# Kernel tuning notes

Measured on AMD Instinct MI355X. Metric: run time of the kernel, lower is better.

## Reference

```python
import jax, jax.numpy as jnp
import numpy as np

N = 50000
E = 800000
HID = 128
EIN = 2 * HID + 1  # h[row] ++ h[col] ++ edge_attr
NC = 3             # n_coords
DIM = 3            # spatial dim
NORM_FACTOR = 100.0
LN_EPS = 1e-5


def layernorm(x, g, b):
    m = jnp.mean(x, axis=-1, keepdims=True)
    v = jnp.mean(jnp.square(x - m), axis=-1, keepdims=True)
    return (x - m) * jax.lax.rsqrt(v + LN_EPS) * g + b


def setup_inputs() -> dict:
    key = jax.random.key(0)
    ks = jax.random.split(key, 12)
    h = jax.random.normal(ks[0], (N, HID), dtype=jnp.float32)
    coord = jax.random.normal(ks[1], (N, NC, DIM), dtype=jnp.float32)
    coord_diff = jax.random.normal(ks[2], (E, NC, DIM), dtype=jnp.float32)
    edge_attr = jax.random.normal(ks[3], (E, 1), dtype=jnp.float32)
    edge_mask = jnp.ones((E, 1), dtype=jnp.float32)
    node_mask = jnp.ones((N, 1, 1), dtype=jnp.float32)
    row = jax.random.randint(ks[4], (E,), 0, N, dtype=jnp.int32)
    col = jax.random.randint(ks[5], (E,), 0, N, dtype=jnp.int32)
    # MLP params (stored [in, out])
    def xavier(k, fi, fo, gain=1.0):
        lim = gain * np.sqrt(6.0 / (fi + fo))
        return jax.random.uniform(k, (fi, fo), dtype=jnp.float32, minval=-lim, maxval=lim)
    W1 = xavier(ks[6], EIN, HID)
    b1 = jnp.zeros((HID,), jnp.float32)
    g1 = jnp.ones((HID,), jnp.float32)
    be1 = jnp.zeros((HID,), jnp.float32)
    W2 = xavier(ks[7], HID, HID)
    b2 = jnp.zeros((HID,), jnp.float32)
    g2 = jnp.ones((HID,), jnp.float32)
    be2 = jnp.zeros((HID,), jnp.float32)
    W3 = xavier(ks[8], HID, NC * NC, gain=0.01)  # final layer, no bias
    return dict(h=h, coord=coord, coord_diff=coord_diff, edge_attr=edge_attr,
                edge_mask=edge_mask, node_mask=node_mask, row=row, col=col,
                W1=W1, b1=b1, g1=g1, be1=be1, W2=W2, b2=b2, g2=g2, be2=be2, W3=W3)


def reference(h, coord, coord_diff, edge_attr, edge_mask, node_mask, row, col,
              W1, b1, g1, be1, W2, b2, g2, be2, W3):
    # gather node feats into edge features: [E, 2*HID + 1]
    x = jnp.concatenate([h[row], h[col], edge_attr], axis=1)
    x = jax.nn.silu(layernorm(x @ W1 + b1, g1, be1))
    x = jax.nn.silu(layernorm(x @ W2 + b2, g2, be2))
    phi = (x @ W3).reshape(-1, NC, NC)               # [E, NC, NC]
    trans = jnp.einsum('ejk,ejl->elk', coord_diff, phi)  # [E, NC, DIM]
    trans = trans * edge_mask[:, None]               # [E,1,1] broadcast
    agg = jax.ops.segment_sum(trans, row, num_segments=coord.shape[0]) / NORM_FACTOR
    return (coord + agg) * node_mask
```

## Files before the change

kernel.cpp:

```cpp
#include <hip/hip_runtime.h>
#include <hip/hip_bf16.h>

#define NN 50000
#define EE 800000

typedef __attribute__((ext_vector_type(8))) short short8;
typedef __attribute__((ext_vector_type(4))) short short4v;
typedef __attribute__((ext_vector_type(4))) float f32x4;

__device__ __forceinline__ float bf2f(ushort u) {
  union { unsigned u; float f; } v; v.u = ((unsigned)u) << 16; return v.f;
}
__device__ __forceinline__ ushort f2bf(float f) {
  union { float f; unsigned u; } v; v.f = f;
  unsigned r = v.u + 0x7FFFu + ((v.u >> 16) & 1u);
  return (ushort)(r >> 16);
}
__device__ __forceinline__ float silu(float v) {
  return v * __builtin_amdgcn_rcpf(1.f + __expf(-v));
}

__global__ void prep_kernel(const float* __restrict__ W1, const float* __restrict__ W2,
                            const float* __restrict__ W3,
                            ushort* __restrict__ W1at, ushort* __restrict__ W1bt,
                            ushort* __restrict__ W2t, ushort* __restrict__ W3t,
                            float* __restrict__ agg) {
  int b = blockIdx.x, tid = threadIdx.x;
  if (b < 200) {
    int i = b * 256 + tid;
    if (i < 16384) {
      int n = i >> 7, k = i & 127;
      W1at[i] = f2bf(W1[k*128 + n]);
    } else if (i < 32768) {
      int j = i - 16384, n = j >> 7, k = j & 127;
      W1bt[j] = f2bf(W1[(k + 128)*128 + n]);
    } else if (i < 49152) {
      int j = i - 32768, n = j >> 7, k = j & 127;
      W2t[j] = f2bf(W2[k*128 + n]);
    } else if (i < 51200) {
      int j = i - 49152, n = j >> 7, k = j & 127;
      W3t[j] = (n < 9) ? f2bf(W3[k*9 + n]) : (ushort)0;
    }
  } else {
    int i = (b - 200) * 256 + tid;
    if (i < NN*9) agg[i] = 0.f;
  }
}

__global__ __launch_bounds__(256, 4)
void node_kernel(const float* __restrict__ h,
                 const ushort* __restrict__ W1at, const ushort* __restrict__ W1bt,
                 const float* __restrict__ b1,
                 ushort* __restrict__ P, ushort* __restrict__ Q) {
  __shared__ __align__(16) ushort smH[64*128];
  const int tid = threadIdx.x;
  const int lane = tid & 63;
  const int w   = tid >> 6;
  const int l15 = lane & 15;
  const int lh  = lane >> 4;
  const int wm  = w >> 1;
  const int wn  = w & 1;
  const int n0  = blockIdx.x * 64;

  {
    int e = tid >> 2, p = tid & 3;
    int nn = n0 + e; if (nn >= NN) nn = NN - 1;
    const float* s = h + (size_t)nn*128 + p*32;
    #pragma unroll
    for (int c = 0; c < 4; ++c) {
      float4 a = *(const float4*)(s + c*8);
      float4 bq = *(const float4*)(s + c*8 + 4);
      short8 v;
      v[0]=f2bf(a.x); v[1]=f2bf(a.y); v[2]=f2bf(a.z); v[3]=f2bf(a.w);
      v[4]=f2bf(bq.x); v[5]=f2bf(bq.y); v[6]=f2bf(bq.z); v[7]=f2bf(bq.w);
      int bo = (e*256 + p*64 + c*16) ^ ((e & 7) << 4);
      *(short8*)((char*)smH + bo) = v;
    }
  }
  __syncthreads();

  const ushort* W = wm ? W1bt : W1at;
  f32x4 acc[4][2] = {};
  #pragma unroll
  for (int k0 = 0; k0 < 4; ++k0) {
    short8 a[4], b[2];
    #pragma unroll
    for (int mf = 0; mf < 4; ++mf)
      a[mf] = *(const short8*)(W + (size_t)(mf*16 + l15)*128 + k0*32 + lh*8);
    #pragma unroll
    for (int nf = 0; nf < 2; ++nf) {
      int e = wn*32 + nf*16 + l15;
      int bo = (e*256 + k0*64 + lh*16) ^ ((e & 7) << 4);
      b[nf] = *(const short8*)((char*)smH + bo);
    }
    #pragma unroll
    for (int mf = 0; mf < 4; ++mf)
      #pragma unroll
      for (int nf = 0; nf < 2; ++nf)
        acc[mf][nf] = __builtin_amdgcn_mfma_f32_16x16x32_bf16(a[mf], b[nf], acc[mf][nf], 0, 0, 0);
  }

  #pragma unroll
  for (int mf = 0; mf < 4; ++mf) {
    float4 bq = *(const float4*)(b1 + mf*16 + lh*4);
    #pragma unroll
    for (int nf = 0; nf < 2; ++nf) {
      int node = n0 + wn*32 + nf*16 + l15;
      if (node < NN) {
        f32x4 r = acc[mf][nf];
        if (wm == 0) { r[0]+=bq.x; r[1]+=bq.y; r[2]+=bq.z; r[3]+=bq.w; }
        ushort* dst = (wm ? Q : P) + (size_t)node*128 + mf*16 + lh*4;
        short4v o; o[0]=f2bf(r[0]); o[1]=f2bf(r[1]); o[2]=f2bf(r[2]); o[3]=f2bf(r[3]);
        *(short4v*)dst = o;
      }
    }
  }
}

__global__ __launch_bounds__(256, 4)
void edge_kernel(const ushort* __restrict__ P, const ushort* __restrict__ Q,
                 const float* __restrict__ w1last,
                 const float* __restrict__ g1, const float* __restrict__ be1,
                 const ushort* __restrict__ W2t, const ushort* __restrict__ W3t,
                 const float* __restrict__ b2, const float* __restrict__ g2, const float* __restrict__ be2,
                 const float* __restrict__ edge_attr, const float* __restrict__ edge_mask,
                 const float* __restrict__ coord_diff,
                 const int* __restrict__ row, const int* __restrict__ col,
                 float* __restrict__ agg) {
  __shared__ __align__(16) char smem[23808];
  ushort* smX   = (ushort*)smem;
  float*  smPhi = (float*)(smem + 16384);
  float*  smCd  = (float*)(smem + 21504);

  const int tid  = threadIdx.x;
  const int lane = tid & 63;
  const int w    = tid >> 6;
  const int l15  = lane & 15;
  const int lh   = lane >> 4;
  const int e0   = blockIdx.x * 64;
  const int we   = w * 16;

  {
    int e = tid >> 2, p = tid & 3;
    int ge = e0 + e;
    int re = row[ge], ce = col[ge];
    float ea = edge_attr[ge];
    const ushort* Pp = P + (size_t)re*128 + p*32;
    const ushort* Qp = Q + (size_t)ce*128 + p*32;
    short8 pa[4], qa[4];
    #pragma unroll
    for (int c = 0; c < 4; ++c) pa[c] = *(const short8*)(Pp + c*8);
    #pragma unroll
    for (int c = 0; c < 4; ++c) qa[c] = *(const short8*)(Qp + c*8);

    if (lane < 36)
      *(float4*)(smCd + we*9 + lane*4) =
          *(const float4*)(coord_diff + (size_t)(e0 + we)*9 + lane*4);

    float v[32]; float s = 0.f, q = 0.f;
    #pragma unroll
    for (int c = 0; c < 4; ++c) {
      float4 wq0 = *(const float4*)(w1last + p*32 + c*8);
      float4 wq1 = *(const float4*)(w1last + p*32 + c*8 + 4);
      #pragma unroll
      for (int j = 0; j < 8; ++j) {
        float wv = (j < 4) ? ((const float*)&wq0)[j] : ((const float*)&wq1)[j-4];
        float t = bf2f((ushort)pa[c][j]) + bf2f((ushort)qa[c][j]) + ea * wv;
        v[c*8 + j] = t; s += t; q += t*t;
      }
    }
    s += __shfl_xor(s, 1, 64); s += __shfl_xor(s, 2, 64);
    q += __shfl_xor(q, 1, 64); q += __shfl_xor(q, 2, 64);
    float m  = s * (1.f/128.f);
    float rs = rsqrtf(q * (1.f/128.f) - m*m + 1e-5f);
    #pragma unroll
    for (int c = 0; c < 4; ++c) {
      float4 gq0 = *(const float4*)(g1 + p*32 + c*8);
      float4 gq1 = *(const float4*)(g1 + p*32 + c*8 + 4);
      float4 bq0 = *(const float4*)(be1 + p*32 + c*8);
      float4 bq1 = *(const float4*)(be1 + p*32 + c*8 + 4);
      short8 o;
      #pragma unroll
      for (int j = 0; j < 8; ++j) {
        float gv = (j < 4) ? ((const float*)&gq0)[j] : ((const float*)&gq1)[j-4];
        float bv = (j < 4) ? ((const float*)&bq0)[j] : ((const float*)&bq1)[j-4];
        float val = (v[c*8+j] - m) * rs * gv + bv;
        o[j] = f2bf(silu(val));
      }
      int bo = (e*256 + p*64 + c*16) ^ ((e & 7) << 4);
      *(short8*)((char*)smX + bo) = o;
    }
  }
  asm volatile("s_waitcnt lgkmcnt(0)" ::: "memory");
  __builtin_amdgcn_sched_barrier(0);

  const int e2 = we + l15;

  f32x4 acc2[8] = {};
  #pragma unroll
  for (int k0 = 0; k0 < 4; ++k0) {
    int bo = (e2*256 + k0*64 + lh*16) ^ ((e2 & 7) << 4);
    short8 bfrag = *(const short8*)((char*)smX + bo);
    #pragma unroll
    for (int mf = 0; mf < 8; ++mf) {
      short8 a = *(const short8*)(W2t + (size_t)(mf*16 + l15)*128 + k0*32 + lh*8);
      acc2[mf] = __builtin_amdgcn_mfma_f32_16x16x32_bf16(a, bfrag, acc2[mf], 0, 0, 0);
    }
  }

  float s2 = 0.f, q2 = 0.f;
  #pragma unroll
  for (int mf = 0; mf < 8; ++mf) {
    float4 bq = *(const float4*)(b2 + mf*16 + lh*4);
    #pragma unroll
    for (int j = 0; j < 4; ++j) {
      float t = acc2[mf][j] + ((const float*)&bq)[j];
      acc2[mf][j] = t; s2 += t; q2 += t*t;
    }
  }
  s2 += __shfl_xor(s2, 16, 64); s2 += __shfl_xor(s2, 32, 64);
  q2 += __shfl_xor(q2, 16, 64); q2 += __shfl_xor(q2, 32, 64);
  {
    float m  = s2 * (1.f/128.f);
    float rs = rsqrtf(q2 * (1.f/128.f) - m*m + 1e-5f);
    #pragma unroll
    for (int mf = 0; mf < 8; ++mf) {
      float4 gq  = *(const float4*)(g2 + mf*16 + lh*4);
      float4 beq = *(const float4*)(be2 + mf*16 + lh*4);
      short4v o;
      #pragma unroll
      for (int j = 0; j < 4; ++j) {
        float val = (acc2[mf][j] - m) * rs * ((const float*)&gq)[j] + ((const float*)&beq)[j];
        o[j] = f2bf(silu(val));
      }
      int bo = (e2*256 + (mf*16 + lh*4)*2) ^ ((e2 & 7) << 4);
      *(short4v*)((char*)smX + bo) = o;
    }
  }
  asm volatile("s_waitcnt lgkmcnt(0)" ::: "memory");
  __builtin_amdgcn_sched_barrier(0);

  {
    f32x4 acc3 = {};
    const ushort* A3 = W3t + (size_t)l15 * 128 + lh*8;
    #pragma unroll
    for (int k0 = 0; k0 < 4; ++k0) {
      short8 a = *(const short8*)(A3 + k0*32);
      int bo = (e2*256 + k0*64 + lh*16) ^ ((e2 & 7) << 4);
      short8 b = *(const short8*)((char*)smX + bo);
      acc3 = __builtin_amdgcn_mfma_f32_16x16x32_bf16(a, b, acc3, 0, 0, 0);
    }
    *(float4*)(smPhi + e2*20 + lh*4) = *(float4*)&acc3;
  }
  asm volatile("s_waitcnt lgkmcnt(0)" ::: "memory");
  __builtin_amdgcn_sched_barrier(0);

  if (lh < 3) {
    int ge = e0 + e2;
    int re = row[ge];
    float em = edge_mask[ge];
    const float* cd = smCd + e2*9;
    const float* ph = smPhi + e2*20;
    int l = lh;
    #pragma unroll
    for (int k = 0; k < 3; ++k) {
      float t = cd[k]*ph[l] + cd[3+k]*ph[3+l] + cd[6+k]*ph[6+l];
      unsafeAtomicAdd(&agg[(size_t)re*9 + l*3 + k], t * em);
    }
  }
}

__global__ void finalize_kernel(const float* __restrict__ coord, const float* __restrict__ node_mask,
                                const float* __restrict__ agg, float* __restrict__ out) {
  int i = blockIdx.x * 256 + threadIdx.x;
  if (i < NN*9) {
    int n = i / 9;
    out[i] = (coord[i] + agg[i] * 0.01f) * node_mask[n];
  }
}

extern "C" void kernel_launch(void* const* d_in, const int* in_sizes, int n_in,
                              void* d_out, int out_size, void* d_ws, size_t ws_size,
                              hipStream_t stream) {
  const float* h          = (const float*)d_in[0];
  const float* coord      = (const float*)d_in[1];
  const float* coord_diff = (const float*)d_in[2];
  const float* edge_attr  = (const float*)d_in[3];
  const float* edge_mask  = (const float*)d_in[4];
  const float* node_mask  = (const float*)d_in[5];
  const int*   rowi       = (const int*)d_in[6];
  const int*   coli       = (const int*)d_in[7];
  const float* W1  = (const float*)d_in[8];
  const float* b1  = (const float*)d_in[9];
  const float* g1  = (const float*)d_in[10];
  const float* be1 = (const float*)d_in[11];
  const float* W2  = (const float*)d_in[12];
  const float* b2  = (const float*)d_in[13];
  const float* g2  = (const float*)d_in[14];
  const float* be2 = (const float*)d_in[15];
  const float* W3  = (const float*)d_in[16];
  const float* w1last = W1 + 256*128;

  char* ws = (char*)d_ws;
  ushort* P    = (ushort*)ws;
  ushort* Q    = (ushort*)(ws + 12800000);
  float*  agg  = (float*)(ws + 25600000);
  ushort* W1at = (ushort*)(ws + 27400192);
  ushort* W1bt = (ushort*)(ws + 27432960);
  ushort* W2t  = (ushort*)(ws + 27465728);
  ushort* W3t  = (ushort*)(ws + 27498496);

  const int nodeBlocks = (NN + 63) / 64;
  const int aggBlocks  = (NN*9 + 255) / 256;

  prep_kernel<<<200 + aggBlocks, 256, 0, stream>>>(W1, W2, W3, W1at, W1bt, W2t, W3t, agg);
  node_kernel<<<nodeBlocks, 256, 0, stream>>>(h, W1at, W1bt, b1, P, Q);
  edge_kernel<<<EE/64, 256, 0, stream>>>(P, Q, w1last, g1, be1, W2t, W3t,
      b2, g2, be2, edge_attr, edge_mask, coord_diff, rowi, coli, agg);
  finalize_kernel<<<aggBlocks, 256, 0, stream>>>(coord, node_mask, agg, (float*)d_out);
}
```

Measured before the change: 554.6 us.

## Make edge kernel persistent per wave with double-buffered gather prefetch

The edge kernel now gives each wave 80 edges, processed as five 16-edge tiles. The P/Q row gathers and coord_diff loads for the next tile are issued into registers before the current tile is computed, so gather latency overlaps the MFMA and LayerNorm work. Each tile is handled by one wave with no block-level sharing, and coord_diff is read straight into registers rather than staged through shared memory. In exchange, register pressure roughly doubles, so launch bounds drop from 4 to 2 blocks per CU, which lowers occupancy.

After: 601.6 us. 8.5% more time.

```diff
diff --git a/kernel.cpp b/kernel.cpp
--- a/kernel.cpp
+++ b/kernel.cpp
@@ -117,7 +117,133 @@
   }
 }
 
-__global__ __launch_bounds__(256, 4)
+__device__ __forceinline__ void compute_tile(
+    const short8* pa, const short8* qa, const float* cdv,
+    float eaT, int rT, float emT,
+    ushort* smX, float* smPhi,
+    const float* __restrict__ w1last,
+    const float* __restrict__ g1, const float* __restrict__ be1,
+    const ushort* __restrict__ W2t, const ushort* __restrict__ W3t,
+    const float* __restrict__ b2, const float* __restrict__ g2,
+    const float* __restrict__ be2,
+    float* __restrict__ agg, int w, int lane)
+{
+  const int l15 = lane & 15, lh = lane >> 4;
+  const int el  = lane >> 2, p = lane & 3;
+  const int e   = w*16 + el;
+  const int e2  = w*16 + l15;
+
+  {
+    float v[32]; float s = 0.f, q = 0.f;
+    #pragma unroll
+    for (int c = 0; c < 4; ++c) {
+      float4 wq0 = *(const float4*)(w1last + p*32 + c*8);
+      float4 wq1 = *(const float4*)(w1last + p*32 + c*8 + 4);
+      #pragma unroll
+      for (int j = 0; j < 8; ++j) {
+        float wv = (j < 4) ? ((const float*)&wq0)[j] : ((const float*)&wq1)[j-4];
+        float t = bf2f((ushort)pa[c][j]) + bf2f((ushort)qa[c][j]) + eaT * wv;
+        v[c*8 + j] = t; s += t; q += t*t;
+      }
+    }
+    s += __shfl_xor(s, 1, 64); s += __shfl_xor(s, 2, 64);
+    q += __shfl_xor(q, 1, 64); q += __shfl_xor(q, 2, 64);
+    float m  = s * (1.f/128.f);
+    float rs = rsqrtf(q * (1.f/128.f) - m*m + 1e-5f);
+    #pragma unroll
+    for (int c = 0; c < 4; ++c) {
+      float4 gq0 = *(const float4*)(g1 + p*32 + c*8);
+      float4 gq1 = *(const float4*)(g1 + p*32 + c*8 + 4);
+      float4 bq0 = *(const float4*)(be1 + p*32 + c*8);
+      float4 bq1 = *(const float4*)(be1 + p*32 + c*8 + 4);
+      short8 o;
+      #pragma unroll
+      for (int j = 0; j < 8; ++j) {
+        float gv = (j < 4) ? ((const float*)&gq0)[j] : ((const float*)&gq1)[j-4];
+        float bv = (j < 4) ? ((const float*)&bq0)[j] : ((const float*)&bq1)[j-4];
+        float val = (v[c*8+j] - m) * rs * gv + bv;
+        o[j] = f2bf(silu(val));
+      }
+      int bo = (e*256 + p*64 + c*16) ^ ((e & 7) << 4);
+      *(short8*)((char*)smX + bo) = o;
+    }
+  }
+  asm volatile("s_waitcnt lgkmcnt(0)" ::: "memory");
+  __builtin_amdgcn_sched_barrier(0);
+
+  {
+    f32x4 acc2[8] = {};
+    #pragma unroll
+    for (int k0 = 0; k0 < 4; ++k0) {
+      int bo = (e2*256 + k0*64 + lh*16) ^ ((e2 & 7) << 4);
+      short8 bfrag = *(const short8*)((char*)smX + bo);
+      #pragma unroll
+      for (int mf = 0; mf < 8; ++mf) {
+        short8 a = *(const short8*)(W2t + (size_t)(mf*16 + l15)*128 + k0*32 + lh*8);
+        acc2[mf] = __builtin_amdgcn_mfma_f32_16x16x32_bf16(a, bfrag, acc2[mf], 0, 0, 0);
+      }
+    }
+    float s2 = 0.f, q2 = 0.f;
+    #pragma unroll
+    for (int mf = 0; mf < 8; ++mf) {
+      float4 bq = *(const float4*)(b2 + mf*16 + lh*4);
+      #pragma unroll
+      for (int j = 0; j < 4; ++j) {
+        float t = acc2[mf][j] + ((const float*)&bq)[j];
+        acc2[mf][j] = t; s2 += t; q2 += t*t;
+      }
+    }
+    s2 += __shfl_xor(s2, 16, 64); s2 += __shfl_xor(s2, 32, 64);
+    q2 += __shfl_xor(q2, 16, 64); q2 += __shfl_xor(q2, 32, 64);
+    float m  = s2 * (1.f/128.f);
+    float rs = rsqrtf(q2 * (1.f/128.f) - m*m + 1e-5f);
+    #pragma unroll
+    for (int mf = 0; mf < 8; ++mf) {
+      float4 gq  = *(const float4*)(g2 + mf*16 + lh*4);
+      float4 beq = *(const float4*)(be2 + mf*16 + lh*4);
+      short4v o;
+      #pragma unroll
+      for (int j = 0; j < 4; ++j) {
+        float val = (acc2[mf][j] - m) * rs * ((const float*)&gq)[j] + ((const float*)&beq)[j];
+        o[j] = f2bf(silu(val));
+      }
+      int bo = (e2*256 + (mf*16 + lh*4)*2) ^ ((e2 & 7) << 4);
+      *(short4v*)((char*)smX + bo) = o;
+    }
+  }
+  asm volatile("s_waitcnt lgkmcnt(0)" ::: "memory");
+  __builtin_amdgcn_sched_barrier(0);
+
+  {
+    f32x4 acc3 = {};
+    const ushort* A3 = W3t + (size_t)l15*128 + lh*8;
+    #pragma unroll
+    for (int k0 = 0; k0 < 4; ++k0) {
+      short8 a = *(const short8*)(A3 + k0*32);
+      int bo = (e2*256 + k0*64 + lh*16) ^ ((e2 & 7) << 4);
+      short8 b = *(const short8*)((char*)smX + bo);
+      acc3 = __builtin_amdgcn_mfma_f32_16x16x32_bf16(a, b, acc3, 0, 0, 0);
+    }
+    *(float4*)(smPhi + e2*20 + lh*4) = *(float4*)&acc3;
+  }
+  asm volatile("s_waitcnt lgkmcnt(0)" ::: "memory");
+  __builtin_amdgcn_sched_barrier(0);
+
+  {
+    int   re = __shfl(rT,  l15 << 2, 64);
+    float em = __shfl(emT, l15 << 2, 64);
+    if (lh < 3) {
+      const float* ph = smPhi + e2*20;
+      #pragma unroll
+      for (int k = 0; k < 3; ++k) {
+        float t = cdv[k]*ph[lh] + cdv[3+k]*ph[3+lh] + cdv[6+k]*ph[6+lh];
+        unsafeAtomicAdd(&agg[(size_t)re*9 + lh*3 + k], t * em);
+      }
+    }
+  }
+}
+
+__global__ __launch_bounds__(256, 2)
 void edge_kernel(const ushort* __restrict__ P, const ushort* __restrict__ Q,
                  const float* __restrict__ w1last,
                  const float* __restrict__ g1, const float* __restrict__ be1,
@@ -127,147 +253,57 @@
                  const float* __restrict__ coord_diff,
                  const int* __restrict__ row, const int* __restrict__ col,
                  float* __restrict__ agg) {
-  __shared__ __align__(16) char smem[23808];
+  __shared__ __align__(16) char smem[21504];
   ushort* smX   = (ushort*)smem;
   float*  smPhi = (float*)(smem + 16384);
-  float*  smCd  = (float*)(smem + 21504);
 
   const int tid  = threadIdx.x;
   const int lane = tid & 63;
   const int w    = tid >> 6;
   const int l15  = lane & 15;
-  const int lh   = lane >> 4;
-  const int e0   = blockIdx.x * 64;
-  const int we   = w * 16;
-
-  {
-    int e = tid >> 2, p = tid & 3;
-    int ge = e0 + e;
-    int re = row[ge], ce = col[ge];
-    float ea = edge_attr[ge];
-    const ushort* Pp = P + (size_t)re*128 + p*32;
-    const ushort* Qp = Q + (size_t)ce*128 + p*32;
-    short8 pa[4], qa[4];
-    #pragma unroll
-    for (int c = 0; c < 4; ++c) pa[c] = *(const short8*)(Pp + c*8);
-    #pragma unroll
-    for (int c = 0; c < 4; ++c) qa[c] = *(const short8*)(Qp + c*8);
-
-    if (lane < 36)
-      *(float4*)(smCd + we*9 + lane*4) =
-          *(const float4*)(coord_diff + (size_t)(e0 + we)*9 + lane*4);
-
-    float v[32]; float s = 0.f, q = 0.f;
-    #pragma unroll
-    for (int c = 0; c < 4; ++c) {
-      float4 wq0 = *(const float4*)(w1last + p*32 + c*8);
-      float4 wq1 = *(const float4*)(w1last + p*32 + c*8 + 4);
-      #pragma unroll
-      for (int j = 0; j < 8; ++j) {
-        float wv = (j < 4) ? ((const float*)&wq0)[j] : ((const float*)&wq1)[j-4];
-        float t = bf2f((ushort)pa[c][j]) + bf2f((ushort)qa[c][j]) + ea * wv;
-        v[c*8 + j] = t; s += t; q += t*t;
-      }
-    }
-    s += __shfl_xor(s, 1, 64); s += __shfl_xor(s, 2, 64);
-    q += __shfl_xor(q, 1, 64); q += __shfl_xor(q, 2, 64);
-    float m  = s * (1.f/128.f);
-    float rs = rsqrtf(q * (1.f/128.f) - m*m + 1e-5f);
-    #pragma unroll
-    for (int c = 0; c < 4; ++c) {
-      float4 gq0 = *(const float4*)(g1 + p*32 + c*8);
-      float4 gq1 = *(const float4*)(g1 + p*32 + c*8 + 4);
-      float4 bq0 = *(const float4*)(be1 + p*32 + c*8);
-      float4 bq1 = *(const float4*)(be1 + p*32 + c*8 + 4);
-      short8 o;
-      #pragma unroll
-      for (int j = 0; j < 8; ++j) {
-        float gv = (j < 4) ? ((const float*)&gq0)[j] : ((const float*)&gq1)[j-4];
-        float bv = (j < 4) ? ((const float*)&bq0)[j] : ((const float*)&bq1)[j-4];
-        float val = (v[c*8+j] - m) * rs * gv + bv;
-        o[j] = f2bf(silu(val));
-      }
-      int bo = (e*256 + p*64 + c*16) ^ ((e & 7) << 4);
-      *(short8*)((char*)smX + bo) = o;
-    }
-  }
-  asm volatile("s_waitcnt lgkmcnt(0)" ::: "memory");
-  __builtin_amdgcn_sched_barrier(0);
-
-  const int e2 = we + l15;
-
-  f32x4 acc2[8] = {};
-  #pragma unroll
-  for (int k0 = 0; k0 < 4; ++k0) {
-    int bo = (e2*256 + k0*64 + lh*16) ^ ((e2 & 7) << 4);
-    short8 bfrag = *(const short8*)((char*)smX + bo);
-    #pragma unroll
-    for (int mf = 0; mf < 8; ++mf) {
-      short8 a = *(const short8*)(W2t + (size_t)(mf*16 + l15)*128 + k0*32 + lh*8);
-      acc2[mf] = __builtin_amdgcn_mfma_f32_16x16x32_bf16(a, bfrag, acc2[mf], 0, 0, 0);
-    }
-  }
-
-  float s2 = 0.f, q2 = 0.f;
-  #pragma unroll
-  for (int mf = 0; mf < 8; ++mf) {
-    float4 bq = *(const float4*)(b2 + mf*16 + lh*4);
-    #pragma unroll
-    for (int j = 0; j < 4; ++j) {
-      float t = acc2[mf][j] + ((const float*)&bq)[j];
-      acc2[mf][j] = t; s2 += t; q2 += t*t;
-    }
-  }
-  s2 += __shfl_xor(s2, 16, 64); s2 += __shfl_xor(s2, 32, 64);
-  q2 += __shfl_xor(q2, 16, 64); q2 += __shfl_xor(q2, 32, 64);
-  {
-    float m  = s2 * (1.f/128.f);
-    float rs = rsqrtf(q2 * (1.f/128.f) - m*m + 1e-5f);
-    #pragma unroll
-    for (int mf = 0; mf < 8; ++mf) {
-      float4 gq  = *(const float4*)(g2 + mf*16 + lh*4);
-      float4 beq = *(const float4*)(be2 + mf*16 + lh*4);
-      short4v o;
-      #pragma unroll
-      for (int j = 0; j < 4; ++j) {
-        float val = (acc2[mf][j] - m) * rs * ((const float*)&gq)[j] + ((const float*)&beq)[j];
-        o[j] = f2bf(silu(val));
-      }
-      int bo = (e2*256 + (mf*16 + lh*4)*2) ^ ((e2 & 7) << 4);
-      *(short4v*)((char*)smX + bo) = o;
-    }
-  }
-  asm volatile("s_waitcnt lgkmcnt(0)" ::: "memory");
-  __builtin_amdgcn_sched_barrier(0);
-
-  {
-    f32x4 acc3 = {};
-    const ushort* A3 = W3t + (size_t)l15 * 128 + lh*8;
-    #pragma unroll
-    for (int k0 = 0; k0 < 4; ++k0) {
-      short8 a = *(const short8*)(A3 + k0*32);
-      int bo = (e2*256 + k0*64 + lh*16) ^ ((e2 & 7) << 4);
-      short8 b = *(const short8*)((char*)smX + bo);
-      acc3 = __builtin_amdgcn_mfma_f32_16x16x32_bf16(a, b, acc3, 0, 0, 0);
-    }
-    *(float4*)(smPhi + e2*20 + lh*4) = *(float4*)&acc3;
-  }
-  asm volatile("s_waitcnt lgkmcnt(0)" ::: "memory");
-  __builtin_amdgcn_sched_barrier(0);
-
-  if (lh < 3) {
-    int ge = e0 + e2;
-    int re = row[ge];
-    float em = edge_mask[ge];
-    const float* cd = smCd + e2*9;
-    const float* ph = smPhi + e2*20;
-    int l = lh;
-    #pragma unroll
-    for (int k = 0; k < 3; ++k) {
-      float t = cd[k]*ph[l] + cd[3+k]*ph[3+l] + cd[6+k]*ph[6+l];
-      unsafeAtomicAdd(&agg[(size_t)re*9 + l*3 + k], t * em);
-    }
-  }
+  const int el   = lane >> 2;
+  const int p    = lane & 3;
+  const int base = (blockIdx.x * 4 + w) * 80;
+
+  int r_[5], c_[5]; float ea_[5], em_[5];
+  short8 paA[4], qaA[4], paB[4], qaB[4];
+  float  cdA[9], cdB[9];
+
+#define LOADRC(t) { int ge = base + (t)*16 + el; \
+  r_[t] = row[ge]; c_[t] = col[ge]; ea_[t] = edge_attr[ge]; em_[t] = edge_mask[ge]; }
+
+#define ISSUE(PAx, QAx, CDx, t) { \
+  const ushort* Pp = P + (size_t)r_[t]*128 + p*32; \
+  const ushort* Qp = Q + (size_t)c_[t]*128 + p*32; \
+  PAx[0] = *(const short8*)Pp;        PAx[1] = *(const short8*)(Pp + 8); \
+  PAx[2] = *(const short8*)(Pp + 16); PAx[3] = *(const short8*)(Pp + 24); \
+  QAx[0] = *(const short8*)Qp;        QAx[1] = *(const short8*)(Qp + 8); \
+  QAx[2] = *(const short8*)(Qp + 16); QAx[3] = *(const short8*)(Qp + 24); \
+  const float* cdp = coord_diff + (size_t)(base + (t)*16 + l15)*9; \
+  CDx[0]=cdp[0]; CDx[1]=cdp[1]; CDx[2]=cdp[2]; CDx[3]=cdp[3]; CDx[4]=cdp[4]; \
+  CDx[5]=cdp[5]; CDx[6]=cdp[6]; CDx[7]=cdp[7]; CDx[8]=cdp[8]; }
+
+#define CT(PAx, QAx, CDx, t) compute_tile(PAx, QAx, CDx, ea_[t], r_[t], em_[t], \
+  smX, smPhi, w1last, g1, be1, W2t, W3t, b2, g2, be2, agg, w, lane);
+
+  LOADRC(0) LOADRC(1)
+  ISSUE(paA, qaA, cdA, 0)
+  LOADRC(2)
+  ISSUE(paB, qaB, cdB, 1)
+  CT(paA, qaA, cdA, 0)
+  LOADRC(3)
+  ISSUE(paA, qaA, cdA, 2)
+  CT(paB, qaB, cdB, 1)
+  LOADRC(4)
+  ISSUE(paB, qaB, cdB, 3)
+  CT(paA, qaA, cdA, 2)
+  ISSUE(paA, qaA, cdA, 4)
+  CT(paB, qaB, cdB, 3)
+  CT(paA, qaA, cdA, 4)
+
+#undef LOADRC
+#undef ISSUE
+#undef CT
 }
 
 __global__ void finalize_kernel(const float* __restrict__ coord, const float* __restrict__ node_mask,
@@ -315,7 +351,7 @@
 
   prep_kernel<<<200 + aggBlocks, 256, 0, stream>>>(W1, W2, W3, W1at, W1bt, W2t, W3t, agg);
   node_kernel<<<nodeBlocks, 256, 0, stream>>>(h, W1at, W1bt, b1, P, Q);
-  edge_kernel<<<EE/64, 256, 0, stream>>>(P, Q, w1last, g1, be1, W2t, W3t,
+  edge_kernel<<<2500, 256, 0, stream>>>(P, Q, w1last, g1, be1, W2t, W3t,
       b2, g2, be2, edge_attr, edge_mask, coord_diff, rowi, coli, agg);
   finalize_kernel<<<aggBlocks, 256, 0, stream>>>(coord, node_mask, agg, (float*)d_out);
 }
```
